# Kernel tuning notes

Hardware: AMD Instinct MI355X
Metric: run time of the kernel (lower is better)

The kernel has to match this reference:

```python
import jax, jax.numpy as jnp
import numpy as np

MAX_DISP = 4          # displacement radius -> 9x9 = 81 output channels
B, C, H, W = 8, 128, 96, 160


def setup_inputs() -> dict:
    key = jax.random.key(0)
    k1, k2 = jax.random.split(key)
    tensorFirst = jax.random.normal(k1, (B, C, H, W), dtype=jnp.float32)
    tensorSecond = jax.random.normal(k2, (B, C, H, W), dtype=jnp.float32)
    return {"tensorFirst": tensorFirst, "tensorSecond": tensorSecond}


def correlation(first, second):
    # first, second: [B, C, H, W]
    b, c, h, w = first.shape
    d = MAX_DISP
    pad = jnp.pad(second, ((0, 0), (0, 0), (d, d), (d, d)))  # [B,C,H+8,W+8]
    inv_c = jnp.asarray(1.0 / c, dtype=first.dtype)
    # channel order: (dy+4)*9 + (dx+4), dx fastest (matches CUDA kernel)
    chans = [
        (first * pad[:, :, dy:dy + h, dx:dx + w]).sum(axis=1) * inv_c
        for dy in range(2 * d + 1)
        for dx in range(2 * d + 1)
    ]
    return jnp.stack(chans, axis=1)  # [B, 81, H, W]


def reference(tensorFirst, tensorSecond):
    return correlation(tensorFirst, tensorSecond)
```

## Files before the change

kernel.cpp:

```cpp
#include <hip/hip_runtime.h>
#include <stdint.h>


typedef __attribute__((ext_vector_type(8))) short bf16x8;
typedef __attribute__((ext_vector_type(4))) float f32x4;

constexpr int Bn = 8, Cn = 128, Hn = 96, Wn = 160;
constexpr int CHS = Hn * Wn;
constexpr int YP = Hn + 8;
constexpr int XPD = Wn + 16;
constexpr size_t SECP_OCTS = (size_t)Bn * YP * XPD * 16;
constexpr size_t SECP_BYTES = SECP_OCTS * 16;

__device__ __forceinline__ uint32_t bf16rne(float f) {
    uint32_t u = __float_as_uint(f);
    return (u + 0x7FFFu + ((u >> 16) & 1u)) >> 16;
}
__device__ __forceinline__ uint32_t pk(float a, float b) {
    return bf16rne(a) | (bf16rne(b) << 16);
}

__global__ __launch_bounds__(256)
void prepass(const float* __restrict__ sec, uint4* __restrict__ secp)
{
    __shared__ float xfer[80 * 130];
    const int h   = blockIdx.x;
    const int yp  = blockIdx.y;
    const int b   = blockIdx.z;
    const int y   = yp - 4;
    const int tid = threadIdx.x;
    const bool live = (y >= 0) && (y < Hn);

    if (live) {
        const float* src = sec + (size_t)b * Cn * CHS + (size_t)y * Wn + h * 80;
        #pragma unroll
        for (int i = 0; i < 10; ++i) {
            int e = tid + i * 256;
            int c = e / 20, x4 = e % 20;
            float4 v = *(const float4*)(src + (size_t)c * CHS + 4 * x4);
            float* d = &xfer[(4 * x4) * 130 + c];
            d[0] = v.x; d[130] = v.y; d[260] = v.z; d[390] = v.w;
        }
    }
    __syncthreads();

    uint4* dst = secp + ((size_t)(b * YP + yp) * XPD) * 16;
    #pragma unroll
    for (int i = 0; i < 6; ++i) {
        int e = tid + i * 256;
        if (e < 88 * 16) {
            int oc = e & 15, xq = e >> 4;
            int xp = h * 88 + xq;
            int x  = xp - 8;
            uint4 o = make_uint4(0u, 0u, 0u, 0u);
            if (live && x >= 0 && x < Wn) {
                const float* p = &xfer[(x - h * 80) * 130 + 8 * oc];
                o.x = pk(p[0], p[1]); o.y = pk(p[2], p[3]);
                o.z = pk(p[4], p[5]); o.w = pk(p[6], p[7]);
            }
            dst[(size_t)xp * 16 + oc] = o;
        }
    }
}

__global__ __launch_bounds__(1024)
void corrmfma(const float* __restrict__ first, const uint4* __restrict__ secp,
              float* __restrict__ out)
{
    __shared__ uint4 smem[16 * 48 * 4];

    const int tid  = threadIdx.x;
    const int w    = tid >> 6;
    const int lane = tid & 63;
    const int quad = lane >> 4;
    const int n16  = lane & 15;
    const int s    = w & 1;
    const int r    = w >> 1;
    const int x0   = blockIdx.x * 32;
    const int y0   = blockIdx.y * 8;
    const int b    = blockIdx.z;
    const int y    = y0 + r;
    const int x0s  = x0 + 16 * s;

    bf16x8 aF[4];
    {
        const float* fp = first + (size_t)b * Cn * CHS + (size_t)y * Wn + x0s + n16;
        #pragma unroll
        for (int kc = 0; kc < 4; ++kc) {
            float f[8];
            #pragma unroll
            for (int j = 0; j < 8; ++j)
                f[j] = fp[(size_t)(32 * kc + 8 * quad + j) * CHS];
            union { uint32_t u[4]; bf16x8 v; } cv;
            cv.u[0] = pk(f[0], f[1]); cv.u[1] = pk(f[2], f[3]);
            cv.u[2] = pk(f[4], f[5]); cv.u[3] = pk(f[6], f[7]);
            aF[kc] = cv.v;
        }
    }

    const uint4* sb = secp + (size_t)b * YP * XPD * 16;
    int gbase[3], lpos[3];
    #pragma unroll
    for (int i = 0; i < 3; ++i) {
        int e = tid + i * 1024;
        int row = e / 192, rem = e % 192;
        int xw = rem >> 2, q = rem & 3;
        gbase[i] = ((y0 + row) * XPD + (x0 + xw)) * 16 + q;
        lpos[i]  = (row * 48 + xw) * 4 + ((q + xw + (xw >> 2)) & 3);
    }

    int bo[2];
    #pragma unroll
    for (int t = 0; t < 2; ++t) {
        int xwr = 16 * (s + t) + n16;
        bo[t] = xwr * 4 + ((quad + xwr + (xwr >> 2)) & 3);
    }

    f32x4 acc[9][2];
    #pragma unroll
    for (int dy = 0; dy < 9; ++dy)
        #pragma unroll
        for (int t = 0; t < 2; ++t)
            acc[dy][t] = (f32x4){0.f, 0.f, 0.f, 0.f};

    uint4 st[3];
    #pragma unroll
    for (int i = 0; i < 3; ++i) st[i] = sb[gbase[i]];

    #pragma unroll
    for (int kc = 0; kc < 4; ++kc) {
        #pragma unroll
        for (int i = 0; i < 3; ++i) smem[lpos[i]] = st[i];
        __syncthreads();
        if (kc < 3) {
            #pragma unroll
            for (int i = 0; i < 3; ++i) st[i] = sb[gbase[i] + 4 * (kc + 1)];
        }
        #pragma unroll
        for (int dy = 0; dy < 9; ++dy) {
            const int rb = (r + dy) * 192;
            #pragma unroll
            for (int t = 0; t < 2; ++t) {
                union { uint4 u; bf16x8 v; } bf;
                bf.u = smem[rb + bo[t]];
                acc[dy][t] = __builtin_amdgcn_mfma_f32_16x16x32_bf16(
                                 aF[kc], bf.v, acc[dy][t], 0, 0, 0);
            }
        }
        __syncthreads();
    }

    const float inv = 1.0f / 128.0f;
    float* ob = out + (size_t)b * 81 * CHS + (size_t)y * Wn + x0s;
    #pragma unroll
    for (int dy = 0; dy < 9; ++dy)
        #pragma unroll
        for (int t = 0; t < 2; ++t)
            #pragma unroll
            for (int reg = 0; reg < 4; ++reg) {
                int mm = quad * 4 + reg;
                int dxc = 16 * t + n16 - mm - 4;
                if (dxc >= 0 && dxc <= 8)
                    ob[(size_t)(dy * 9 + dxc) * CHS + mm] = acc[dy][t][reg] * inv;
            }
}

constexpr int FTW = 32, FTH = 16, FNT = 128;
constexpr int FHR = FTH + 2, FHC4 = 12, FPITCH = 48;
constexpr int FSLOTS = FHR * FHC4;

__global__ __launch_bounds__(FNT, 2)
void corr3_fb(const float* __restrict__ first, const float* __restrict__ second,
              float* __restrict__ out)
{
    __shared__ float lds[2][FHR * FPITCH];
    const int tid = threadIdx.x;
    const int tx = tid & 7, ty = tid >> 3;
    const int x0 = blockIdx.x * FTW, y0 = blockIdx.y * FTH;
    const int b = blockIdx.z / 3, g = blockIdx.z % 3;
    const int row0 = y0 + 3 * g - 4;
    const int e0 = tid, e1 = tid + FNT;
    const int r0 = e0 / FHC4, c40 = e0 % FHC4;
    const int r1 = e1 / FHC4, c41 = e1 % FHC4;
    const int gy0 = row0 + r0, gy1 = row0 + r1;
    const int gx0 = x0 - 8 + c40 * 4, gx1 = x0 - 8 + c41 * 4;
    const bool s1ok = (e1 < FSLOTS);
    const bool v0 = (gy0 >= 0) & (gy0 < Hn) & (gx0 >= 0) & (gx0 < Wn);
    const bool v1 = s1ok & (gy1 >= 0) & (gy1 < Hn) & (gx1 >= 0) & (gx1 < Wn);
    const int go0 = gy0 * Wn + gx0, go1 = gy1 * Wn + gx1;
    const int lo0 = r0 * FPITCH + c40 * 4, lo1 = r1 * FPITCH + c41 * 4;
    const float* secb = second + (size_t)b * Cn * CHS;
    const float* fb = first + (size_t)b * Cn * CHS + (y0 + ty) * Wn + x0 + tx * 4;
    float acc[3][9][4] = {};
    {
        float4 a0 = make_float4(0, 0, 0, 0), a1 = make_float4(0, 0, 0, 0);
        if (v0) a0 = *(const float4*)(secb + go0);
        if (v1) a1 = *(const float4*)(secb + go1);
        *(float4*)&lds[0][lo0] = a0;
        if (s1ok) *(float4*)&lds[0][lo1] = a1;
    }
    __syncthreads();
    #pragma unroll 1
    for (int c = 0; c < Cn; ++c) {
        const int cur = c & 1;
        float4 nn0 = make_float4(0, 0, 0, 0), nn1 = make_float4(0, 0, 0, 0);
        const bool hn = (c + 1 < Cn);
        if (hn) {
            const float* sp = secb + (c + 1) * CHS;
            if (v0) nn0 = *(const float4*)(sp + go0);
            if (v1) nn1 = *(const float4*)(sp + go1);
        }
        float4 fv = *(const float4*)(fb + c * CHS);
        float fa[4] = {fv.x, fv.y, fv.z, fv.w};
        #pragma unroll
        for (int d = 0; d < 3; ++d) {
            const float* rp = &lds[cur][(ty + d) * FPITCH + tx * 4 + 4];
            float4 w0 = *(const float4*)(rp + 0);
            float4 w1 = *(const float4*)(rp + 4);
            float4 w2 = *(const float4*)(rp + 8);
            float wv[12] = {w0.x, w0.y, w0.z, w0.w, w1.x, w1.y, w1.z, w1.w,
                            w2.x, w2.y, w2.z, w2.w};
            #pragma unroll
            for (int dx = 0; dx < 9; ++dx)
                #pragma unroll
                for (int p = 0; p < 4; ++p)
                    acc[d][dx][p] = fmaf(fa[p], wv[dx + p], acc[d][dx][p]);
        }
        if (hn) {
            *(float4*)&lds[1 - cur][lo0] = nn0;
            if (s1ok) *(float4*)&lds[1 - cur][lo1] = nn1;
        }
        __syncthreads();
    }
    const float invc = 1.0f / (float)Cn;
    float* ob = out + (size_t)b * 81 * CHS + (y0 + ty) * Wn + x0 + tx * 4;
    #pragma unroll
    for (int d = 0; d < 3; ++d)
        #pragma unroll
        for (int dx = 0; dx < 9; ++dx) {
            const int chn = (3 * g + d) * 9 + dx;
            float4 o = make_float4(acc[d][dx][0] * invc, acc[d][dx][1] * invc,
                                   acc[d][dx][2] * invc, acc[d][dx][3] * invc);
            *(float4*)(ob + (size_t)chn * CHS) = o;
        }
}

extern "C" void kernel_launch(void* const* d_in, const int* in_sizes, int n_in,
                              void* d_out, int out_size, void* d_ws, size_t ws_size,
                              hipStream_t stream) {
    const float* first  = (const float*)d_in[0];
    const float* second = (const float*)d_in[1];
    float* out = (float*)d_out;

    if (ws_size >= SECP_BYTES) {
        uint4* secp = (uint4*)d_ws;
        prepass<<<dim3(2, YP, Bn), dim3(256, 1, 1), 0, stream>>>(second, secp);
        corrmfma<<<dim3(Wn / 32, Hn / 8, Bn), dim3(1024, 1, 1), 0, stream>>>(
            first, secp, out);
    } else {
        corr3_fb<<<dim3(Wn / FTW, Hn / FTH, Bn * 3), dim3(FNT, 1, 1), 0, stream>>>(
            first, second, out);
    }
}
```

Measured before the change: 219.4 us.

## Fuse bf16 packing of second into MFMA kernel and stage output through LDS

```diff
diff --git a/kernel.cpp b/kernel.cpp
--- a/kernel.cpp
+++ b/kernel.cpp
@@ -7,10 +7,6 @@
 
 constexpr int Bn = 8, Cn = 128, Hn = 96, Wn = 160;
 constexpr int CHS = Hn * Wn;
-constexpr int YP = Hn + 8;
-constexpr int XPD = Wn + 16;
-constexpr size_t SECP_OCTS = (size_t)Bn * YP * XPD * 16;
-constexpr size_t SECP_BYTES = SECP_OCTS * 16;
 
 __device__ __forceinline__ uint32_t bf16rne(float f) {
     uint32_t u = __float_as_uint(f);
@@ -20,52 +16,9 @@
     return bf16rne(a) | (bf16rne(b) << 16);
 }
 
-__global__ __launch_bounds__(256)
-void prepass(const float* __restrict__ sec, uint4* __restrict__ secp)
-{
-    __shared__ float xfer[80 * 130];
-    const int h   = blockIdx.x;
-    const int yp  = blockIdx.y;
-    const int b   = blockIdx.z;
-    const int y   = yp - 4;
-    const int tid = threadIdx.x;
-    const bool live = (y >= 0) && (y < Hn);
-
-    if (live) {
-        const float* src = sec + (size_t)b * Cn * CHS + (size_t)y * Wn + h * 80;
-        #pragma unroll
-        for (int i = 0; i < 10; ++i) {
-            int e = tid + i * 256;
-            int c = e / 20, x4 = e % 20;
-            float4 v = *(const float4*)(src + (size_t)c * CHS + 4 * x4);
-            float* d = &xfer[(4 * x4) * 130 + c];
-            d[0] = v.x; d[130] = v.y; d[260] = v.z; d[390] = v.w;
-        }
-    }
-    __syncthreads();
-
-    uint4* dst = secp + ((size_t)(b * YP + yp) * XPD) * 16;
-    #pragma unroll
-    for (int i = 0; i < 6; ++i) {
-        int e = tid + i * 256;
-        if (e < 88 * 16) {
-            int oc = e & 15, xq = e >> 4;
-            int xp = h * 88 + xq;
-            int x  = xp - 8;
-            uint4 o = make_uint4(0u, 0u, 0u, 0u);
-            if (live && x >= 0 && x < Wn) {
-                const float* p = &xfer[(x - h * 80) * 130 + 8 * oc];
-                o.x = pk(p[0], p[1]); o.y = pk(p[2], p[3]);
-                o.z = pk(p[4], p[5]); o.w = pk(p[6], p[7]);
-            }
-            dst[(size_t)xp * 16 + oc] = o;
-        }
-    }
-}
-
 __global__ __launch_bounds__(1024)
-void corrmfma(const float* __restrict__ first, const uint4* __restrict__ secp,
-              float* __restrict__ out)
+void corrfused(const float* __restrict__ first, const float* __restrict__ second,
+               float* __restrict__ out)
 {
     __shared__ uint4 smem[16 * 48 * 4];
 
@@ -98,15 +51,18 @@
         }
     }
 
-    const uint4* sb = secp + (size_t)b * YP * XPD * 16;
-    int gbase[3], lpos[3];
+    const float* sb = second + (size_t)b * Cn * CHS;
+    int goff[3], lpos[3];
+    bool val[3];
     #pragma unroll
     for (int i = 0; i < 3; ++i) {
         int e = tid + i * 1024;
         int row = e / 192, rem = e % 192;
         int xw = rem >> 2, q = rem & 3;
-        gbase[i] = ((y0 + row) * XPD + (x0 + xw)) * 16 + q;
-        lpos[i]  = (row * 48 + xw) * 4 + ((q + xw + (xw >> 2)) & 3);
+        int gy = y0 + row - 4, gx = x0 + xw - 8;
+        val[i]  = (gy >= 0) && (gy < Hn) && (gx >= 0) && (gx < Wn);
+        goff[i] = val[i] ? (8 * q * CHS + gy * Wn + gx) : 0;
+        lpos[i] = (row * 48 + xw) * 4 + ((q + xw + (xw >> 2)) & 3);
     }
 
     int bo[2];
@@ -123,18 +79,30 @@
         for (int t = 0; t < 2; ++t)
             acc[dy][t] = (f32x4){0.f, 0.f, 0.f, 0.f};
 
-    uint4 st[3];
+    float fr[3][8];
     #pragma unroll
-    for (int i = 0; i < 3; ++i) st[i] = sb[gbase[i]];
+    for (int i = 0; i < 3; ++i)
+        #pragma unroll
+        for (int j = 0; j < 8; ++j)
+            fr[i][j] = sb[goff[i] + (size_t)j * CHS];
 
     #pragma unroll
     for (int kc = 0; kc < 4; ++kc) {
         #pragma unroll
-        for (int i = 0; i < 3; ++i) smem[lpos[i]] = st[i];
+        for (int i = 0; i < 3; ++i) {
+            uint4 o;
+            o.x = pk(fr[i][0], fr[i][1]); o.y = pk(fr[i][2], fr[i][3]);
+            o.z = pk(fr[i][4], fr[i][5]); o.w = pk(fr[i][6], fr[i][7]);
+            if (!val[i]) o = make_uint4(0u, 0u, 0u, 0u);
+            smem[lpos[i]] = o;
+        }
         __syncthreads();
         if (kc < 3) {
             #pragma unroll
-            for (int i = 0; i < 3; ++i) st[i] = sb[gbase[i] + 4 * (kc + 1)];
+            for (int i = 0; i < 3; ++i)
+                #pragma unroll
+                for (int j = 0; j < 8; ++j)
+                    fr[i][j] = sb[goff[i] + (size_t)(32 * (kc + 1) + j) * CHS];
         }
         #pragma unroll
         for (int dy = 0; dy < 9; ++dy) {
@@ -151,114 +119,44 @@
     }
 
     const float inv = 1.0f / 128.0f;
+    float* sm = (float*)smem;
     float* ob = out + (size_t)b * 81 * CHS + (size_t)y * Wn + x0s;
+    const int wb = w * 540;
     #pragma unroll
-    for (int dy = 0; dy < 9; ++dy)
+    for (int ck = 0; ck < 3; ++ck) {
         #pragma unroll
-        for (int t = 0; t < 2; ++t)
+        for (int d = 0; d < 3; ++d)
             #pragma unroll
-            for (int reg = 0; reg < 4; ++reg) {
-                int mm = quad * 4 + reg;
-                int dxc = 16 * t + n16 - mm - 4;
-                if (dxc >= 0 && dxc <= 8)
-                    ob[(size_t)(dy * 9 + dxc) * CHS + mm] = acc[dy][t][reg] * inv;
+            for (int t = 0; t < 2; ++t)
+                #pragma unroll
+                for (int reg = 0; reg < 4; ++reg) {
+                    int mm  = quad * 4 + reg;
+                    int dxc = 16 * t + n16 - mm - 4;
+                    if (dxc >= 0 && dxc <= 8)
+                        sm[wb + (d * 9 + dxc) * 20 + mm] = acc[ck * 3 + d][t][reg] * inv;
+                }
+        __syncthreads();
+        #pragma unroll
+        for (int ii = 0; ii < 2; ++ii) {
+            int slot = lane + ii * 64;
+            if (slot < 108) {
+                int chn = slot >> 2, g = slot & 3;
+                float4 v = *(const float4*)&sm[wb + chn * 20 + 4 * g];
+                int ch = (ck * 3 + chn / 9) * 9 + chn % 9;
+                *(float4*)(ob + (size_t)ch * CHS + 4 * g) = v;
             }
-}
-
-constexpr int FTW = 32, FTH = 16, FNT = 128;
-constexpr int FHR = FTH + 2, FHC4 = 12, FPITCH = 48;
-constexpr int FSLOTS = FHR * FHC4;
-
-__global__ __launch_bounds__(FNT, 2)
-void corr3_fb(const float* __restrict__ first, const float* __restrict__ second,
-              float* __restrict__ out)
-{
-    __shared__ float lds[2][FHR * FPITCH];
-    const int tid = threadIdx.x;
-    const int tx = tid & 7, ty = tid >> 3;
-    const int x0 = blockIdx.x * FTW, y0 = blockIdx.y * FTH;
-    const int b = blockIdx.z / 3, g = blockIdx.z % 3;
-    const int row0 = y0 + 3 * g - 4;
-    const int e0 = tid, e1 = tid + FNT;
-    const int r0 = e0 / FHC4, c40 = e0 % FHC4;
-    const int r1 = e1 / FHC4, c41 = e1 % FHC4;
-    const int gy0 = row0 + r0, gy1 = row0 + r1;
-    const int gx0 = x0 - 8 + c40 * 4, gx1 = x0 - 8 + c41 * 4;
-    const bool s1ok = (e1 < FSLOTS);
-    const bool v0 = (gy0 >= 0) & (gy0 < Hn) & (gx0 >= 0) & (gx0 < Wn);
-    const bool v1 = s1ok & (gy1 >= 0) & (gy1 < Hn) & (gx1 >= 0) & (gx1 < Wn);
-    const int go0 = gy0 * Wn + gx0, go1 = gy1 * Wn + gx1;
-    const int lo0 = r0 * FPITCH + c40 * 4, lo1 = r1 * FPITCH + c41 * 4;
-    const float* secb = second + (size_t)b * Cn * CHS;
-    const float* fb = first + (size_t)b * Cn * CHS + (y0 + ty) * Wn + x0 + tx * 4;
-    float acc[3][9][4] = {};
-    {
-        float4 a0 = make_float4(0, 0, 0, 0), a1 = make_float4(0, 0, 0, 0);
-        if (v0) a0 = *(const float4*)(secb + go0);
-        if (v1) a1 = *(const float4*)(secb + go1);
-        *(float4*)&lds[0][lo0] = a0;
-        if (s1ok) *(float4*)&lds[0][lo1] = a1;
-    }
-    __syncthreads();
-    #pragma unroll 1
-    for (int c = 0; c < Cn; ++c) {
-        const int cur = c & 1;
-        float4 nn0 = make_float4(0, 0, 0, 0), nn1 = make_float4(0, 0, 0, 0);
-        const bool hn = (c + 1 < Cn);
-        if (hn) {
-            const float* sp = secb + (c + 1) * CHS;
-            if (v0) nn0 = *(const float4*)(sp + go0);
-            if (v1) nn1 = *(const float4*)(sp + go1);
-        }
-        float4 fv = *(const float4*)(fb + c * CHS);
-        float fa[4] = {fv.x, fv.y, fv.z, fv.w};
-        #pragma unroll
-        for (int d = 0; d < 3; ++d) {
-            const float* rp = &lds[cur][(ty + d) * FPITCH + tx * 4 + 4];
-            float4 w0 = *(const float4*)(rp + 0);
-            float4 w1 = *(const float4*)(rp + 4);
-            float4 w2 = *(const float4*)(rp + 8);
-            float wv[12] = {w0.x, w0.y, w0.z, w0.w, w1.x, w1.y, w1.z, w1.w,
-                            w2.x, w2.y, w2.z, w2.w};
-            #pragma unroll
-            for (int dx = 0; dx < 9; ++dx)
-                #pragma unroll
-                for (int p = 0; p < 4; ++p)
-                    acc[d][dx][p] = fmaf(fa[p], wv[dx + p], acc[d][dx][p]);
-        }
-        if (hn) {
-            *(float4*)&lds[1 - cur][lo0] = nn0;
-            if (s1ok) *(float4*)&lds[1 - cur][lo1] = nn1;
         }
         __syncthreads();
     }
-    const float invc = 1.0f / (float)Cn;
-    float* ob = out + (size_t)b * 81 * CHS + (y0 + ty) * Wn + x0 + tx * 4;
-    #pragma unroll
-    for (int d = 0; d < 3; ++d)
-        #pragma unroll
-        for (int dx = 0; dx < 9; ++dx) {
-            const int chn = (3 * g + d) * 9 + dx;
-            float4 o = make_float4(acc[d][dx][0] * invc, acc[d][dx][1] * invc,
-                                   acc[d][dx][2] * invc, acc[d][dx][3] * invc);
-            *(float4*)(ob + (size_t)chn * CHS) = o;
-        }
 }
 
 extern "C" void kernel_launch(void* const* d_in, const int* in_sizes, int n_in,
                               void* d_out, int out_size, void* d_ws, size_t ws_size,
                               hipStream_t stream) {
+    (void)in_sizes; (void)n_in; (void)d_ws; (void)ws_size; (void)out_size;
     const float* first  = (const float*)d_in[0];
     const float* second = (const float*)d_in[1];
     float* out = (float*)d_out;
-
-    if (ws_size >= SECP_BYTES) {
-        uint4* secp = (uint4*)d_ws;
-        prepass<<<dim3(2, YP, Bn), dim3(256, 1, 1), 0, stream>>>(second, secp);
-        corrmfma<<<dim3(Wn / 32, Hn / 8, Bn), dim3(1024, 1, 1), 0, stream>>>(
-            first, secp, out);
-    } else {
-        corr3_fb<<<dim3(Wn / FTW, Hn / FTH, Bn * 3), dim3(FNT, 1, 1), 0, stream>>>(
-            first, second, out);
-    }
+    corrfused<<<dim3(Wn / 32, Hn / 8, Bn), dim3(1024, 1, 1), 0, stream>>>(
+        first, second, out);
 }
```

Result: faster. 204.4 us (-6.8%).
